# Optimization experiments

Hardware: AMD Instinct MI355X
Metric: run time of the kernel (lower is better)

Reference implementation:

```python
import jax, jax.numpy as jnp
import numpy as np

N, E, C, L = 50000, 800000, 64, 3  # nodes, edges, channels, message-passing layers
EPS = 1e-5  # torch.nn.LayerNorm default eps


def _mlp(h, W0, b0, W1, b1, W2, b2, g, beta):
    # MLP(input, hidden=[C, C], output=C) with ReLU between linears, LayerNorm at end
    h = jax.nn.relu(h @ W0 + b0)
    h = jax.nn.relu(h @ W1 + b1)
    h = h @ W2 + b2
    mu = jnp.mean(h, axis=-1, keepdims=True)
    var = jnp.var(h, axis=-1, keepdims=True)
    return (h - mu) * jax.lax.rsqrt(var + EPS) * g + beta


def setup_inputs() -> dict:
    key = jax.random.key(0)
    ks = jax.random.split(key, 12)
    def w(k, shape, fan_in):
        return (jax.random.normal(k, shape, jnp.float32) / np.float32(np.sqrt(fan_in)))
    return {
        "x": jax.random.normal(ks[0], (N, C), jnp.float32),
        "e": jax.random.normal(ks[1], (E, C), jnp.float32),
        "edge_index": jax.random.randint(ks[2], (2, E), 0, N),
        # edge_updater MLP params, stacked over L layers
        "ew0": w(ks[3], (L, 3 * C, C), 3 * C), "eb0": jnp.zeros((L, C), jnp.float32),
        "ew1": w(ks[4], (L, C, C), C),         "eb1": jnp.zeros((L, C), jnp.float32),
        "ew2": w(ks[5], (L, C, C), C),         "eb2": jnp.zeros((L, C), jnp.float32),
        "eg": jnp.ones((L, C), jnp.float32),   "ebt": jnp.zeros((L, C), jnp.float32),
        # node_updater MLP params
        "nw0": w(ks[6], (L, 2 * C, C), 2 * C), "nb0": jnp.zeros((L, C), jnp.float32),
        "nw1": w(ks[7], (L, C, C), C),         "nb1": jnp.zeros((L, C), jnp.float32),
        "nw2": w(ks[8], (L, C, C), C),         "nb2": jnp.zeros((L, C), jnp.float32),
        "ng": jnp.ones((L, C), jnp.float32),   "nbt": jnp.zeros((L, C), jnp.float32),
    }


def reference(x, e, edge_index, ew0, eb0, ew1, eb1, ew2, eb2, eg, ebt,
              nw0, nb0, nw1, nb1, nw2, nb2, ng, nbt):
    src, dst = edge_index[0], edge_index[1]
    for i in range(L):
        # e += edge_updater(cat(x_src, x_dst, e))
        e = e + _mlp(jnp.concatenate([x[src], x[dst], e], axis=1),
                     ew0[i], eb0[i], ew1[i], eb1[i], ew2[i], eb2[i], eg[i], ebt[i])
        # EdgeAggregation(aggr='add'): scatter-add edge features at target nodes
        agg = jax.ops.segment_sum(e, dst, num_segments=N)
        # x += node_updater(cat(x, agg))
        x = x + _mlp(jnp.concatenate([x, agg], axis=1),
                     nw0[i], nb0[i], nw1[i], nb1[i], nw2[i], nb2[i], ng[i], nbt[i])
    return (x, e)
```

## Files before the change

### kernel.cpp

```cpp
#include <hip/hip_runtime.h>

#define CH 64

using bf16x8 = __attribute__((ext_vector_type(8))) short;
using f32x4  = __attribute__((ext_vector_type(4))) float;

__device__ __forceinline__ unsigned short f2bf(float f) {
  unsigned int u = __float_as_uint(f);
  u = (u + 0x7FFFu + ((u >> 16) & 1u)) >> 16;
  return (unsigned short)u;
}

#define E0S 200
#define S64 72
#define N0S 136

#define EW0_L 0
#define EW1_L 12800
#define EW2_L 17408
#define EW_TOT 22016
#define EH0_L 22016
#define EH1_L 34816
#define E_LDS 39424

#define NW0_L 0
#define NW1_L 8704
#define NW2_L 13312
#define NW_TOT 17920
#define NH0_L 17920
#define NH1_L 26624
#define N_LDS 31232

#define WS_NW 66048
#define WS_AGG_BYTES 262144

__global__ void prep_w(const float* __restrict__ ew0, const float* __restrict__ ew1,
                       const float* __restrict__ ew2, const float* __restrict__ nw0,
                       const float* __restrict__ nw1, const float* __restrict__ nw2,
                       unsigned short* __restrict__ ws) {
  int i = blockIdx.x * 256 + threadIdx.x;
  if (i < 36864) {
    int l = i / 12288, r = i % 12288, k = r / 64, n = r % 64;
    ws[l * EW_TOT + EW0_L + n * E0S + k] = f2bf(ew0[i]);
  } else if (i < 49152) {
    int j = i - 36864, l = j / 4096, r = j % 4096, k = r / 64, n = r % 64;
    ws[l * EW_TOT + EW1_L + n * S64 + k] = f2bf(ew1[j]);
  } else if (i < 61440) {
    int j = i - 49152, l = j / 4096, r = j % 4096, k = r / 64, n = r % 64;
    ws[l * EW_TOT + EW2_L + n * S64 + k] = f2bf(ew2[j]);
  } else if (i < 86016) {
    int j = i - 61440, l = j / 8192, r = j % 8192, k = r / 64, n = r % 64;
    ws[WS_NW + l * NW_TOT + NW0_L + n * N0S + k] = f2bf(nw0[j]);
  } else if (i < 98304) {
    int j = i - 86016, l = j / 4096, r = j % 4096, k = r / 64, n = r % 64;
    ws[WS_NW + l * NW_TOT + NW1_L + n * S64 + k] = f2bf(nw1[j]);
  } else if (i < 110592) {
    int j = i - 98304, l = j / 4096, r = j % 4096, k = r / 64, n = r % 64;
    ws[WS_NW + l * NW_TOT + NW2_L + n * S64 + k] = f2bf(nw2[j]);
  }
}

__global__ __launch_bounds__(256, 2)
void edge_kernel(const float* x, const float* e_in, float* e_out,
                 const int* __restrict__ src, const int* __restrict__ dst,
                 const unsigned short* __restrict__ wg,
                 const float* __restrict__ b0, const float* __restrict__ b1,
                 const float* __restrict__ b2, const float* __restrict__ gam,
                 const float* __restrict__ bet, float* agg, int nE) {
  __shared__ unsigned short lds[E_LDS];
  const int tid = threadIdx.x;
  {
    const uint4* s = (const uint4*)wg;
    uint4* d4 = (uint4*)lds;
    for (int i = tid; i < EW_TOT / 8; i += 256) d4[i] = s[i];
  }
  __syncthreads();

  const int wave = tid >> 6, lane = tid & 63;
  const int quad = lane >> 4, l15 = lane & 15;
  const int h0o = EH0_L + wave * 3200;
  const int h1o = EH1_L + wave * 1152;

  float b0c[4], b1c[4], b2c[4], gc[4], btc[4];
#pragma unroll
  for (int j = 0; j < 4; ++j) {
    int col = j * 16 + l15;
    b0c[j] = b0[col]; b1c[j] = b1[col]; b2c[j] = b2[col];
    gc[j] = gam[col]; btc[j] = bet[col];
  }

  for (int base = blockIdx.x * 64; base < nE; base += gridDim.x * 64) {
    const int ebase = base + wave * 16;
#pragma unroll
    for (int p = 0; p < 4; ++p) {
      int el = p * 4 + quad;
      int eidx = ebase + el;
      int s = src[eidx], d = dst[eidx];
      float4 vs = *(const float4*)(x + (size_t)s * CH + l15 * 4);
      float4 vd = *(const float4*)(x + (size_t)d * CH + l15 * 4);
      float4 ve = *(const float4*)(e_in + (size_t)eidx * CH + l15 * 4);
      ushort4 us; us.x = f2bf(vs.x); us.y = f2bf(vs.y); us.z = f2bf(vs.z); us.w = f2bf(vs.w);
      ushort4 ud; ud.x = f2bf(vd.x); ud.y = f2bf(vd.y); ud.z = f2bf(vd.z); ud.w = f2bf(vd.w);
      ushort4 ue; ue.x = f2bf(ve.x); ue.y = f2bf(ve.y); ue.z = f2bf(ve.z); ue.w = f2bf(ve.w);
      *(ushort4*)(lds + h0o + el * E0S + l15 * 4)       = us;
      *(ushort4*)(lds + h0o + el * E0S + 64 + l15 * 4)  = ud;
      *(ushort4*)(lds + h0o + el * E0S + 128 + l15 * 4) = ue;
    }
    f32x4 acc0[4];
#pragma unroll
    for (int j = 0; j < 4; ++j) acc0[j] = (f32x4){0.f, 0.f, 0.f, 0.f};
#pragma unroll
    for (int t = 0; t < 6; ++t) {
      bf16x8 a = *(const bf16x8*)(lds + h0o + l15 * E0S + t * 32 + quad * 8);
#pragma unroll
      for (int j = 0; j < 4; ++j) {
        bf16x8 b = *(const bf16x8*)(lds + EW0_L + (j * 16 + l15) * E0S + t * 32 + quad * 8);
        acc0[j] = __builtin_amdgcn_mfma_f32_16x16x32_bf16(a, b, acc0[j], 0, 0, 0);
      }
    }
#pragma unroll
    for (int j = 0; j < 4; ++j) {
      int col = j * 16 + l15;
#pragma unroll
      for (int r = 0; r < 4; ++r) {
        float v = fmaxf(acc0[j][r] + b0c[j], 0.f);
        lds[h1o + (quad * 4 + r) * S64 + col] = f2bf(v);
      }
    }
    f32x4 acc1[4];
#pragma unroll
    for (int j = 0; j < 4; ++j) acc1[j] = (f32x4){0.f, 0.f, 0.f, 0.f};
#pragma unroll
    for (int t = 0; t < 2; ++t) {
      bf16x8 a = *(const bf16x8*)(lds + h1o + l15 * S64 + t * 32 + quad * 8);
#pragma unroll
      for (int j = 0; j < 4; ++j) {
        bf16x8 b = *(const bf16x8*)(lds + EW1_L + (j * 16 + l15) * S64 + t * 32 + quad * 8);
        acc1[j] = __builtin_amdgcn_mfma_f32_16x16x32_bf16(a, b, acc1[j], 0, 0, 0);
      }
    }
#pragma unroll
    for (int j = 0; j < 4; ++j) {
      int col = j * 16 + l15;
#pragma unroll
      for (int r = 0; r < 4; ++r) {
        float v = fmaxf(acc1[j][r] + b1c[j], 0.f);
        lds[h0o + (quad * 4 + r) * S64 + col] = f2bf(v);
      }
    }
    f32x4 acc2[4];
#pragma unroll
    for (int j = 0; j < 4; ++j) acc2[j] = (f32x4){0.f, 0.f, 0.f, 0.f};
#pragma unroll
    for (int t = 0; t < 2; ++t) {
      bf16x8 a = *(const bf16x8*)(lds + h0o + l15 * S64 + t * 32 + quad * 8);
#pragma unroll
      for (int j = 0; j < 4; ++j) {
        bf16x8 b = *(const bf16x8*)(lds + EW2_L + (j * 16 + l15) * S64 + t * 32 + quad * 8);
        acc2[j] = __builtin_amdgcn_mfma_f32_16x16x32_bf16(a, b, acc2[j], 0, 0, 0);
      }
    }
    float vv[4][4], s1[4], s2[4];
#pragma unroll
    for (int r = 0; r < 4; ++r) { s1[r] = 0.f; s2[r] = 0.f; }
#pragma unroll
    for (int j = 0; j < 4; ++j)
#pragma unroll
      for (int r = 0; r < 4; ++r) {
        float v = acc2[j][r] + b2c[j];
        vv[j][r] = v; s1[r] += v; s2[r] += v * v;
      }
#pragma unroll
    for (int m = 1; m < 16; m <<= 1)
#pragma unroll
      for (int r = 0; r < 4; ++r) {
        s1[r] += __shfl_xor(s1[r], m, 64);
        s2[r] += __shfl_xor(s2[r], m, 64);
      }
#pragma unroll
    for (int r = 0; r < 4; ++r) {
      int eidx = ebase + quad * 4 + r;
      float mean = s1[r] * 0.015625f;
      float var = s2[r] * 0.015625f - mean * mean;
      float rstd = rsqrtf(var + 1e-5f);
      int dnode = dst[eidx];
      float* aggrow = agg + (size_t)dnode * CH;
      const float* ein_row = e_in + (size_t)eidx * CH;
      float* eout_row = e_out + (size_t)eidx * CH;
#pragma unroll
      for (int j = 0; j < 4; ++j) {
        int col = j * 16 + l15;
        float y = (vv[j][r] - mean) * rstd * gc[j] + btc[j];
        float out = ein_row[col] + y;
        eout_row[col] = out;
        atomicAdd(aggrow + col, out);
      }
    }
  }
}

__global__ __launch_bounds__(256, 2)
void node_kernel(const float* x_in, const float* __restrict__ agg_in,
                 const unsigned short* __restrict__ wg,
                 const float* __restrict__ b0, const float* __restrict__ b1,
                 const float* __restrict__ b2, const float* __restrict__ gam,
                 const float* __restrict__ bet, float* x_out, int nN) {
  __shared__ unsigned short lds[N_LDS];
  const int tid = threadIdx.x;
  {
    const uint4* s = (const uint4*)wg;
    uint4* d4 = (uint4*)lds;
    for (int i = tid; i < NW_TOT / 8; i += 256) d4[i] = s[i];
  }
  __syncthreads();

  const int wave = tid >> 6, lane = tid & 63;
  const int quad = lane >> 4, l15 = lane & 15;
  const int nbase = (blockIdx.x * 4 + wave) * 16;
  if (nbase >= nN) return;
  const int h0o = NH0_L + wave * 2176;
  const int h1o = NH1_L + wave * 1152;

  float b0c[4], b1c[4], b2c[4], gc[4], btc[4];
#pragma unroll
  for (int j = 0; j < 4; ++j) {
    int col = j * 16 + l15;
    b0c[j] = b0[col]; b1c[j] = b1[col]; b2c[j] = b2[col];
    gc[j] = gam[col]; btc[j] = bet[col];
  }

#pragma unroll
  for (int p = 0; p < 4; ++p) {
    int nl = p * 4 + quad;
    int node = nbase + nl;
    float4 vx = *(const float4*)(x_in + (size_t)node * CH + l15 * 4);
    float4 va = *(const float4*)(agg_in + (size_t)node * CH + l15 * 4);
    ushort4 ux; ux.x = f2bf(vx.x); ux.y = f2bf(vx.y); ux.z = f2bf(vx.z); ux.w = f2bf(vx.w);
    ushort4 ua; ua.x = f2bf(va.x); ua.y = f2bf(va.y); ua.z = f2bf(va.z); ua.w = f2bf(va.w);
    *(ushort4*)(lds + h0o + nl * N0S + l15 * 4)      = ux;
    *(ushort4*)(lds + h0o + nl * N0S + 64 + l15 * 4) = ua;
  }
  f32x4 acc0[4];
#pragma unroll
  for (int j = 0; j < 4; ++j) acc0[j] = (f32x4){0.f, 0.f, 0.f, 0.f};
#pragma unroll
  for (int t = 0; t < 4; ++t) {
    bf16x8 a = *(const bf16x8*)(lds + h0o + l15 * N0S + t * 32 + quad * 8);
#pragma unroll
    for (int j = 0; j < 4; ++j) {
      bf16x8 b = *(const bf16x8*)(lds + NW0_L + (j * 16 + l15) * N0S + t * 32 + quad * 8);
      acc0[j] = __builtin_amdgcn_mfma_f32_16x16x32_bf16(a, b, acc0[j], 0, 0, 0);
    }
  }
#pragma unroll
  for (int j = 0; j < 4; ++j) {
    int col = j * 16 + l15;
#pragma unroll
    for (int r = 0; r < 4; ++r) {
      float v = fmaxf(acc0[j][r] + b0c[j], 0.f);
      lds[h1o + (quad * 4 + r) * S64 + col] = f2bf(v);
    }
  }
  f32x4 acc1[4];
#pragma unroll
  for (int j = 0; j < 4; ++j) acc1[j] = (f32x4){0.f, 0.f, 0.f, 0.f};
#pragma unroll
  for (int t = 0; t < 2; ++t) {
    bf16x8 a = *(const bf16x8*)(lds + h1o + l15 * S64 + t * 32 + quad * 8);
#pragma unroll
    for (int j = 0; j < 4; ++j) {
      bf16x8 b = *(const bf16x8*)(lds + NW1_L + (j * 16 + l15) * S64 + t * 32 + quad * 8);
      acc1[j] = __builtin_amdgcn_mfma_f32_16x16x32_bf16(a, b, acc1[j], 0, 0, 0);
    }
  }
#pragma unroll
  for (int j = 0; j < 4; ++j) {
    int col = j * 16 + l15;
#pragma unroll
    for (int r = 0; r < 4; ++r) {
      float v = fmaxf(acc1[j][r] + b1c[j], 0.f);
      lds[h0o + (quad * 4 + r) * S64 + col] = f2bf(v);
    }
  }
  f32x4 acc2[4];
#pragma unroll
  for (int j = 0; j < 4; ++j) acc2[j] = (f32x4){0.f, 0.f, 0.f, 0.f};
#pragma unroll
  for (int t = 0; t < 2; ++t) {
    bf16x8 a = *(const bf16x8*)(lds + h0o + l15 * S64 + t * 32 + quad * 8);
#pragma unroll
    for (int j = 0; j < 4; ++j) {
      bf16x8 b = *(const bf16x8*)(lds + NW2_L + (j * 16 + l15) * S64 + t * 32 + quad * 8);
      acc2[j] = __builtin_amdgcn_mfma_f32_16x16x32_bf16(a, b, acc2[j], 0, 0, 0);
    }
  }
  float vv[4][4], s1[4], s2[4];
#pragma unroll
  for (int r = 0; r < 4; ++r) { s1[r] = 0.f; s2[r] = 0.f; }
#pragma unroll
  for (int j = 0; j < 4; ++j)
#pragma unroll
    for (int r = 0; r < 4; ++r) {
      float v = acc2[j][r] + b2c[j];
      vv[j][r] = v; s1[r] += v; s2[r] += v * v;
    }
#pragma unroll
  for (int m = 1; m < 16; m <<= 1)
#pragma unroll
    for (int r = 0; r < 4; ++r) {
      s1[r] += __shfl_xor(s1[r], m, 64);
      s2[r] += __shfl_xor(s2[r], m, 64);
    }
#pragma unroll
  for (int r = 0; r < 4; ++r) {
    int node = nbase + quad * 4 + r;
    float mean = s1[r] * 0.015625f;
    float var = s2[r] * 0.015625f - mean * mean;
    float rstd = rsqrtf(var + 1e-5f);
    const float* xin_row = x_in + (size_t)node * CH;
    float* xout_row = x_out + (size_t)node * CH;
#pragma unroll
    for (int j = 0; j < 4; ++j) {
      int col = j * 16 + l15;
      float y = (vv[j][r] - mean) * rstd * gc[j] + btc[j];
      xout_row[col] = xin_row[col] + y;
    }
  }
}

extern "C" void kernel_launch(void* const* d_in, const int* in_sizes, int n_in,
                              void* d_out, int out_size, void* d_ws, size_t ws_size,
                              hipStream_t stream) {
  const float* x0 = (const float*)d_in[0];
  const float* e0 = (const float*)d_in[1];
  const int* ei  = (const int*)d_in[2];
  const float* ew0 = (const float*)d_in[3];
  const float* eb0 = (const float*)d_in[4];
  const float* ew1 = (const float*)d_in[5];
  const float* eb1 = (const float*)d_in[6];
  const float* ew2 = (const float*)d_in[7];
  const float* eb2 = (const float*)d_in[8];
  const float* eg  = (const float*)d_in[9];
  const float* ebt = (const float*)d_in[10];
  const float* nw0 = (const float*)d_in[11];
  const float* nb0 = (const float*)d_in[12];
  const float* nw1 = (const float*)d_in[13];
  const float* nb1 = (const float*)d_in[14];
  const float* nw2 = (const float*)d_in[15];
  const float* nb2 = (const float*)d_in[16];
  const float* ng  = (const float*)d_in[17];
  const float* nbt = (const float*)d_in[18];

  const int N = in_sizes[0] / CH;
  const int E = in_sizes[1] / CH;
  const int* src = ei;
  const int* dst = ei + E;

  float* xout = (float*)d_out;
  float* eout = (float*)d_out + (size_t)N * CH;

  unsigned short* wsu = (unsigned short*)d_ws;
  float* agg = (float*)((char*)d_ws + WS_AGG_BYTES);

  prep_w<<<432, 256, 0, stream>>>(ew0, ew1, ew2, nw0, nw1, nw2, wsu);

  for (int l = 0; l < 3; ++l) {
    hipMemsetAsync(agg, 0, (size_t)N * CH * sizeof(float), stream);
    const float* xin = (l == 0) ? x0 : xout;
    const float* einp = (l == 0) ? e0 : eout;
    edge_kernel<<<512, 256, 0, stream>>>(
        xin, einp, eout, src, dst, wsu + l * EW_TOT,
        eb0 + l * CH, eb1 + l * CH, eb2 + l * CH, eg + l * CH, ebt + l * CH,
        agg, E);
    node_kernel<<<(N / 16 + 3) / 4, 256, 0, stream>>>(
        xin, agg, wsu + WS_NW + l * NW_TOT,
        nb0 + l * CH, nb1 + l * CH, nb2 + l * CH, ng + l * CH, nbt + l * CH,
        xout, N);
  }
}
```

Baseline: 1.154 ms.

## Replace atomic scatter-add aggregation with CSR gather-based segment sum

Builds a CSR grouping of edges by destination once per call (histogram, single-block scan, atomic scatter of edge ids), then sums edge features per node in a separate gather kernel instead of float atomicAdd inside the edge kernel. This removes 51M float atomics per layer and the per-layer memset of the aggregation buffer. In exchange it adds an extra full read of the edge features per layer, plus random row gathers and a serial single-block scan over the nodes. Because edge ids within a node land in nondeterministic order, the float summation order still varies between runs.

```diff
diff --git a/kernel.cpp b/kernel.cpp
--- a/kernel.cpp
+++ b/kernel.cpp
@@ -32,7 +32,10 @@
 #define N_LDS 31232
 
 #define WS_NW 66048
-#define WS_AGG_BYTES 262144
+#define WS_AGG_B    262144
+#define WS_ROWPTR_B 13062144
+#define WS_NEXT_B   13262208
+#define WS_EID_B    13462208
 
 __global__ void prep_w(const float* __restrict__ ew0, const float* __restrict__ ew1,
                        const float* __restrict__ ew2, const float* __restrict__ nw0,
@@ -60,13 +63,72 @@
   }
 }
 
+__global__ void hist_k(const int* __restrict__ dst, int* __restrict__ counts, int nE) {
+  int i = blockIdx.x * 256 + threadIdx.x;
+  if (i < nE) atomicAdd(counts + dst[i], 1);
+}
+
+__global__ void scan_k(const int* __restrict__ counts, int* __restrict__ row_ptr,
+                       int* __restrict__ next, int n) {
+  __shared__ int wsum[16];
+  __shared__ int chunk_tot;
+  __shared__ int base_sh;
+  const int tid = threadIdx.x, lane = tid & 63, wv = tid >> 6;
+  if (tid == 0) { base_sh = 0; row_ptr[0] = 0; }
+  __syncthreads();
+  for (int start = 0; start < n; start += 4096) {
+    int idx = start + tid * 4;
+    int v[4], s = 0;
+#pragma unroll
+    for (int k = 0; k < 4; ++k) { v[k] = (idx + k < n) ? counts[idx + k] : 0; s += v[k]; }
+    int incl = s;
+#pragma unroll
+    for (int off = 1; off < 64; off <<= 1) {
+      int t = __shfl_up(incl, off, 64);
+      if (lane >= off) incl += t;
+    }
+    if (lane == 63) wsum[wv] = incl;
+    __syncthreads();
+    if (wv == 0 && lane < 16) {
+      int w = wsum[lane];
+      int wincl = w;
+#pragma unroll
+      for (int off = 1; off < 16; off <<= 1) {
+        int t = __shfl_up(wincl, off, 16);
+        if (lane >= off) wincl += t;
+      }
+      if (lane == 15) chunk_tot = wincl;
+      wsum[lane] = wincl - w;
+    }
+    __syncthreads();
+    int run = base_sh + wsum[wv] + (incl - s);
+#pragma unroll
+    for (int k = 0; k < 4; ++k) {
+      int i = idx + k;
+      if (i < n) { next[i] = run; run += v[k]; row_ptr[i + 1] = run; }
+    }
+    __syncthreads();
+    if (tid == 0) base_sh += chunk_tot;
+    __syncthreads();
+  }
+}
+
+__global__ void scatter_k(const int* __restrict__ dst, int* __restrict__ next,
+                          int* __restrict__ eid, int nE) {
+  int i = blockIdx.x * 256 + threadIdx.x;
+  if (i < nE) {
+    int p = atomicAdd(next + dst[i], 1);
+    eid[p] = i;
+  }
+}
+
 __global__ __launch_bounds__(256, 2)
 void edge_kernel(const float* x, const float* e_in, float* e_out,
                  const int* __restrict__ src, const int* __restrict__ dst,
                  const unsigned short* __restrict__ wg,
                  const float* __restrict__ b0, const float* __restrict__ b1,
                  const float* __restrict__ b2, const float* __restrict__ gam,
-                 const float* __restrict__ bet, float* agg, int nE) {
+                 const float* __restrict__ bet, int nE) {
   __shared__ unsigned short lds[E_LDS];
   const int tid = threadIdx.x;
   {
@@ -183,20 +245,36 @@
       float mean = s1[r] * 0.015625f;
       float var = s2[r] * 0.015625f - mean * mean;
       float rstd = rsqrtf(var + 1e-5f);
-      int dnode = dst[eidx];
-      float* aggrow = agg + (size_t)dnode * CH;
       const float* ein_row = e_in + (size_t)eidx * CH;
       float* eout_row = e_out + (size_t)eidx * CH;
 #pragma unroll
       for (int j = 0; j < 4; ++j) {
         int col = j * 16 + l15;
         float y = (vv[j][r] - mean) * rstd * gc[j] + btc[j];
-        float out = ein_row[col] + y;
-        eout_row[col] = out;
-        atomicAdd(aggrow + col, out);
-      }
-    }
-  }
+        eout_row[col] = ein_row[col] + y;
+      }
+    }
+  }
+}
+
+__global__ __launch_bounds__(256)
+void agg_kernel(const float* __restrict__ e, const int* __restrict__ row_ptr,
+                const int* __restrict__ eid, float* __restrict__ agg, int nN) {
+  int node = blockIdx.x * 4 + (threadIdx.x >> 6);
+  int lane = threadIdx.x & 63;
+  if (node >= nN) return;
+  int r0 = row_ptr[node], r1 = row_ptr[node + 1];
+  float s0 = 0.f, s1 = 0.f, s2 = 0.f, s3 = 0.f;
+  int i = r0;
+  for (; i + 4 <= r1; i += 4) {
+    int e0 = eid[i], e1 = eid[i + 1], e2 = eid[i + 2], e3 = eid[i + 3];
+    s0 += e[(size_t)e0 * CH + lane];
+    s1 += e[(size_t)e1 * CH + lane];
+    s2 += e[(size_t)e2 * CH + lane];
+    s3 += e[(size_t)e3 * CH + lane];
+  }
+  for (; i < r1; ++i) s0 += e[(size_t)eid[i] * CH + lane];
+  agg[(size_t)node * CH + lane] = (s0 + s1) + (s2 + s3);
 }
 
 __global__ __launch_bounds__(256, 2)
@@ -360,18 +438,25 @@
   float* eout = (float*)d_out + (size_t)N * CH;
 
   unsigned short* wsu = (unsigned short*)d_ws;
-  float* agg = (float*)((char*)d_ws + WS_AGG_BYTES);
+  float* agg    = (float*)((char*)d_ws + WS_AGG_B);
+  int* row_ptr  = (int*)((char*)d_ws + WS_ROWPTR_B);
+  int* nxt      = (int*)((char*)d_ws + WS_NEXT_B);
+  int* eid      = (int*)((char*)d_ws + WS_EID_B);
 
   prep_w<<<432, 256, 0, stream>>>(ew0, ew1, ew2, nw0, nw1, nw2, wsu);
 
+  hipMemsetAsync(nxt, 0, (size_t)N * sizeof(int), stream);
+  hist_k<<<(E + 255) / 256, 256, 0, stream>>>(dst, nxt, E);
+  scan_k<<<1, 1024, 0, stream>>>(nxt, row_ptr, nxt, N);
+  scatter_k<<<(E + 255) / 256, 256, 0, stream>>>(dst, nxt, eid, E);
+
   for (int l = 0; l < 3; ++l) {
-    hipMemsetAsync(agg, 0, (size_t)N * CH * sizeof(float), stream);
     const float* xin = (l == 0) ? x0 : xout;
     const float* einp = (l == 0) ? e0 : eout;
     edge_kernel<<<512, 256, 0, stream>>>(
         xin, einp, eout, src, dst, wsu + l * EW_TOT,
-        eb0 + l * CH, eb1 + l * CH, eb2 + l * CH, eg + l * CH, ebt + l * CH,
-        agg, E);
+        eb0 + l * CH, eb1 + l * CH, eb2 + l * CH, eg + l * CH, ebt + l * CH, E);
+    agg_kernel<<<(N + 3) / 4, 256, 0, stream>>>(eout, row_ptr, eid, agg, N);
     node_kernel<<<(N / 16 + 3) / 4, 256, 0, stream>>>(
         xin, agg, wsu + WS_NW + l * NW_TOT,
         nb0 + l * CH, nb1 + l * CH, nb2 + l * CH, ng + l * CH, nbt + l * CH,
```

Result: no change. 1.132 ms (-2.0%).
